# Kernel tuning notes

Measured on AMD Instinct MI355X. Metric: run time of the kernel, lower is better.

The kernel has to match this reference:

```python
import jax, jax.numpy as jnp
import numpy as np

N_CELL = 66
N_SUB = 29934
N = N_CELL + N_SUB  # 30000 nodes
F = 256
E_HALF = 480000
K = 3
LAYERS = 2
BN_EPS = 1e-5


def setup_inputs() -> dict:
    key = jax.random.key(0)
    ks = jax.random.split(key, 8)
    cell_feat = jax.random.normal(ks[0], (N_CELL, F), dtype=jnp.float32)
    sub_feat = jax.random.normal(ks[1], (N_SUB, F), dtype=jnp.float32)
    # interaction_edge builds a symmetric directed edge list: (a,b) and (b,a)
    src = jax.random.randint(ks[2], (E_HALF,), 0, N)
    dst = jax.random.randint(ks[3], (E_HALF,), 0, N)
    edge_index = jnp.stack([jnp.concatenate([src, dst]),
                            jnp.concatenate([dst, src])], axis=0)
    ew_half = jax.random.uniform(ks[4], (E_HALF,), dtype=jnp.float32, minval=0.1, maxval=1.0)
    edge_weight = jnp.concatenate([ew_half, ew_half])
    glorot = np.sqrt(6.0 / (F + F))
    W1 = jax.random.uniform(ks[5], (F, F), dtype=jnp.float32, minval=-glorot, maxval=glorot)
    W2 = jax.random.uniform(ks[6], (F, F), dtype=jnp.float32, minval=-glorot, maxval=glorot)
    b1 = jnp.zeros((F,), jnp.float32)
    b2 = jnp.zeros((F,), jnp.float32)
    prelu_w = jnp.full((F,), 0.25, jnp.float32)  # PReLU default init
    gamma = jnp.ones((F,), jnp.float32)
    beta = jnp.zeros((F,), jnp.float32)
    return {"cell_feat": cell_feat, "sub_feat": sub_feat,
            "edge_index": edge_index, "edge_weight": edge_weight,
            "W1": W1, "b1": b1, "W2": W2, "b2": b2,
            "prelu_w": prelu_w, "gamma": gamma, "beta": beta}


def _gcn_norm(edge_index, edge_weight, n):
    # SGConv's gcn_norm: add self-loops (weight 1), symmetric degree normalization
    loop = jnp.arange(n)
    row = jnp.concatenate([edge_index[0], loop])  # source j
    col = jnp.concatenate([edge_index[1], loop])  # target i
    ew = jnp.concatenate([edge_weight, jnp.ones((n,), edge_weight.dtype)])
    deg = jax.ops.segment_sum(ew, col, num_segments=n)
    dinv = jnp.where(deg > 0, jax.lax.rsqrt(deg), 0.0)
    norm = dinv[row] * ew * dinv[col]
    return row, col, norm


def _sgconv(x, row, col, norm, W, b, n):
    # K-hop propagation: x <- A_hat^K x, then linear
    for _ in range(K):
        x = jax.ops.segment_sum(norm[:, None] * x[row], col, num_segments=n)
    return x @ W.T + b


def _prelu_bn(x, prelu_w, gamma, beta):
    x = jnp.where(x >= 0, x, prelu_w * x)
    mean = jnp.mean(x, axis=0)
    var = jnp.mean(jnp.square(x - mean), axis=0)  # biased, training-mode BN
    return gamma * (x - mean) * jax.lax.rsqrt(var + BN_EPS) + beta


def reference(cell_feat, sub_feat, edge_index, edge_weight,
              W1, b1, W2, b2, prelu_w, gamma, beta):
    x = jnp.concatenate([cell_feat, sub_feat], axis=0)  # [N, F]
    n = x.shape[0]
    row, col, norm = _gcn_norm(edge_index, edge_weight, n)
    for W, b in ((W1, b1), (W2, b2)):
        x = _sgconv(x, row, col, norm, W, b, n)
        x = _prelu_bn(x, prelu_w, gamma, beta)
    return x[:N_CELL, :], x[N_CELL:, :]
```

## Files before the change

### kernel.cpp

```cpp
#include <hip/hip_runtime.h>
#include <hip/hip_bf16.h>

constexpr int NN    = 30000;
constexpr int NCELL = 66;
constexpr int NF    = 256;
constexpr int CAP   = 80;
constexpr float EPS = 1e-5f;

using bf16x8 = __attribute__((ext_vector_type(8))) short;
using f32x4  = __attribute__((ext_vector_type(4))) float;

__device__ __forceinline__ float bf2f(unsigned short u) {
    return __uint_as_float(((unsigned)u) << 16);
}
__device__ __forceinline__ unsigned short f2bf(float f) {
    __hip_bfloat16 h = __float2bfloat16(f);
    return *reinterpret_cast<unsigned short*>(&h);
}
__device__ __forceinline__ void acc8(float* acc, float4 u, float w) {
    unsigned a = __float_as_uint(u.x), b = __float_as_uint(u.y);
    unsigned c = __float_as_uint(u.z), d = __float_as_uint(u.w);
    acc[0] += w * __uint_as_float(a << 16);
    acc[1] += w * __uint_as_float(a & 0xffff0000u);
    acc[2] += w * __uint_as_float(b << 16);
    acc[3] += w * __uint_as_float(b & 0xffff0000u);
    acc[4] += w * __uint_as_float(c << 16);
    acc[5] += w * __uint_as_float(c & 0xffff0000u);
    acc[6] += w * __uint_as_float(d << 16);
    acc[7] += w * __uint_as_float(d & 0xffff0000u);
}
__device__ __forceinline__ void edge_meta(const unsigned long long* p, int& r, float& w) {
    unsigned long long v = *p;
    r = (int)(unsigned)(v & 0xffffffffull);
    w = (float)(unsigned)(v >> 32) * (1.0f / 16777216.0f);
}

__global__ void k_init(int* fill, float* sums) {
    int i = blockIdx.x * 256 + threadIdx.x;
    if (i < NN) fill[i] = 0;
    if (i < 2 * NF) sums[i] = 0.0f;
}

__global__ void k_zero_stats(float* sums) {
    int i = threadIdx.x;
    if (i < 2 * NF) sums[i] = 0.0f;
}

__global__ void k_cvtw(const float4* __restrict__ W, ushort4* __restrict__ Wh) {
    int idx = blockIdx.x * 256 + threadIdx.x;
    if (idx >= NF * NF / 4) return;
    float4 v = W[idx];
    ushort4 o;
    o.x = f2bf(v.x); o.y = f2bf(v.y); o.z = f2bf(v.z); o.w = f2bf(v.w);
    Wh[idx] = o;
}

__global__ void k_scatter(const int* __restrict__ ei, const float* __restrict__ ew,
                          int* fill, unsigned long long* __restrict__ bkt, int E) {
    int e = blockIdx.x * 256 + threadIdx.x;
    if (e >= E) return;
    int row = ei[e];
    int col = ei[E + e];
    unsigned q = __float2uint_rn(ew[e] * 16777216.0f);
    int pos = atomicAdd(&fill[col], 1);
    unsigned long long v = ((unsigned long long)q << 32) | (unsigned)row;
    __builtin_nontemporal_store(v, &bkt[(size_t)col * CAP + pos]);
}

__global__ void k_deg(const unsigned long long* __restrict__ bkt, const int* __restrict__ fill,
                      float* __restrict__ s1, float* __restrict__ s2) {
    int i = blockIdx.x * 256 + threadIdx.x;
    if (i >= NN) return;
    int cnt = fill[i];
    unsigned sq = 0;
    const unsigned long long* p = bkt + (size_t)i * CAP;
    for (int e = 0; e < cnt; e++) sq += (unsigned)(p[e] >> 32);
    float deg = 1.0f + (float)sq * (1.0f / 16777216.0f);
    float di = rsqrtf(deg);
    s2[i] = di;
    s1[i] = di * di;
}

__global__ void k_concat_h(const float4* __restrict__ cell, const float4* __restrict__ sub,
                           const float* __restrict__ dinv, ushort4* __restrict__ xh) {
    int idx = blockIdx.x * 256 + threadIdx.x;
    if (idx >= NN * (NF / 4)) return;
    const int CELL4 = NCELL * (NF / 4);
    float4 v = (idx < CELL4) ? cell[idx] : sub[idx - CELL4];
    float di = dinv[idx >> 6];
    ushort4 o;
    o.x = f2bf(v.x * di); o.y = f2bf(v.y * di);
    o.z = f2bf(v.z * di); o.w = f2bf(v.w * di);
    xh[idx] = o;
}

__global__ __launch_bounds__(256) void k_prop(const ushort* __restrict__ xin,
                                              ushort* __restrict__ xout,
                                              const int* __restrict__ fill,
                                              const unsigned long long* __restrict__ bkt,
                                              const float* __restrict__ scale) {
    int n = blockIdx.x * 4 + (threadIdx.x >> 6);
    int lane = threadIdx.x & 63;
    int half = lane >> 5;
    int fb = lane & 31;
    const float4* xrow = (const float4*)xin;
    const unsigned long long* base = bkt + (size_t)n * CAP;
    int cnt = fill[n];
    float acc[8];
    #pragma unroll
    for (int i = 0; i < 8; i++) acc[i] = 0.f;
    int steps = cnt >> 1;
    int it = 0;
    int e = half;
    for (; it + 8 <= steps; it += 8, e += 16) {
        int r0, r1, r2, r3, r4, r5, r6, r7;
        float w0, w1, w2, w3, w4, w5, w6, w7;
        edge_meta(base + e,      r0, w0);
        edge_meta(base + e + 2,  r1, w1);
        edge_meta(base + e + 4,  r2, w2);
        edge_meta(base + e + 6,  r3, w3);
        edge_meta(base + e + 8,  r4, w4);
        edge_meta(base + e + 10, r5, w5);
        edge_meta(base + e + 12, r6, w6);
        edge_meta(base + e + 14, r7, w7);
        float4 u0 = xrow[r0 * 32 + fb];
        float4 u1 = xrow[r1 * 32 + fb];
        float4 u2 = xrow[r2 * 32 + fb];
        float4 u3 = xrow[r3 * 32 + fb];
        float4 u4 = xrow[r4 * 32 + fb];
        float4 u5 = xrow[r5 * 32 + fb];
        float4 u6 = xrow[r6 * 32 + fb];
        float4 u7 = xrow[r7 * 32 + fb];
        acc8(acc, u0, w0); acc8(acc, u1, w1); acc8(acc, u2, w2); acc8(acc, u3, w3);
        acc8(acc, u4, w4); acc8(acc, u5, w5); acc8(acc, u6, w6); acc8(acc, u7, w7);
    }
    for (; it + 4 <= steps; it += 4, e += 8) {
        int r0, r1, r2, r3; float w0, w1, w2, w3;
        edge_meta(base + e,     r0, w0);
        edge_meta(base + e + 2, r1, w1);
        edge_meta(base + e + 4, r2, w2);
        edge_meta(base + e + 6, r3, w3);
        float4 u0 = xrow[r0 * 32 + fb];
        float4 u1 = xrow[r1 * 32 + fb];
        float4 u2 = xrow[r2 * 32 + fb];
        float4 u3 = xrow[r3 * 32 + fb];
        acc8(acc, u0, w0); acc8(acc, u1, w1); acc8(acc, u2, w2); acc8(acc, u3, w3);
    }
    for (; it < steps; ++it, e += 2) {
        int r0; float w0;
        edge_meta(base + e, r0, w0);
        float4 u0 = xrow[r0 * 32 + fb];
        acc8(acc, u0, w0);
    }
    if ((cnt & 1) && half == 0) {
        int r0; float w0;
        edge_meta(base + cnt - 1, r0, w0);
        float4 u0 = xrow[r0 * 32 + fb];
        acc8(acc, u0, w0);
    }
    #pragma unroll
    for (int i = 0; i < 8; i++) acc[i] += __shfl_xor(acc[i], 32);
    if (half == 0) {
        float4 u = xrow[n * 32 + fb];
        acc8(acc, u, 1.0f);
        float sc = scale[n];
        #pragma unroll
        for (int i = 0; i < 8; i++) acc[i] *= sc;
        unsigned p0 = ((unsigned)f2bf(acc[1]) << 16) | f2bf(acc[0]);
        unsigned p1 = ((unsigned)f2bf(acc[3]) << 16) | f2bf(acc[2]);
        unsigned p2 = ((unsigned)f2bf(acc[5]) << 16) | f2bf(acc[4]);
        unsigned p3 = ((unsigned)f2bf(acc[7]) << 16) | f2bf(acc[6]);
        float4 o;
        o.x = __uint_as_float(p0); o.y = __uint_as_float(p1);
        o.z = __uint_as_float(p2); o.w = __uint_as_float(p3);
        ((float4*)xout)[n * 32 + fb] = o;
    }
}

__global__ __launch_bounds__(256) void k_gemm_fused(const short* __restrict__ A,
                                                    const short* __restrict__ B,
                                                    const float* __restrict__ bias,
                                                    const float* __restrict__ pw,
                                                    float* __restrict__ y,
                                                    float* __restrict__ sums) {
    constexpr int RT = NN / 16;
    int w    = threadIdx.x >> 6;
    int lane = threadIdx.x & 63;
    int rt   = blockIdx.x * 4 + w;
    int ml   = lane & 15;
    int q    = lane >> 4;
    bool valid = rt < RT;
    __shared__ float red[2][4][NF];
    f32x4 acc[16];
    #pragma unroll
    for (int i = 0; i < 16; i++) acc[i] = (f32x4){0.f, 0.f, 0.f, 0.f};
    if (valid) {
        const short* arow = A + (rt * 16 + ml) * NF + q * 8;
        #pragma unroll
        for (int ks = 0; ks < 8; ks++) {
            bf16x8 a = *(const bf16x8*)(arow + ks * 32);
            #pragma unroll
            for (int nt = 0; nt < 16; nt++) {
                bf16x8 b = *(const bf16x8*)(B + (nt * 16 + ml) * NF + ks * 32 + q * 8);
                acc[nt] = __builtin_amdgcn_mfma_f32_16x16x32_bf16(a, b, acc[nt], 0, 0, 0);
            }
        }
    }
    #pragma unroll
    for (int nt = 0; nt < 16; nt++) {
        int col = nt * 16 + ml;
        float s = 0.f, s2 = 0.f;
        if (valid) {
            float bb = bias[col];
            float pc = pw[col];
            #pragma unroll
            for (int r = 0; r < 4; r++) {
                float v = acc[nt][r] + bb;
                v = (v >= 0.f) ? v : pc * v;
                s += v; s2 += v * v;
                y[(rt * 16 + q * 4 + r) * NF + col] = v;
            }
        }
        s  += __shfl_xor(s, 16);  s  += __shfl_xor(s, 32);
        s2 += __shfl_xor(s2, 16); s2 += __shfl_xor(s2, 32);
        if (lane < 16) { red[0][w][col] = s; red[1][w][col] = s2; }
    }
    __syncthreads();
    int t = threadIdx.x;
    float v0 = red[0][0][t] + red[0][1][t] + red[0][2][t] + red[0][3][t];
    float v1 = red[1][0][t] + red[1][1][t] + red[1][2][t] + red[1][3][t];
    atomicAdd(&sums[t], v0);
    atomicAdd(&sums[NF + t], v1);
}

__global__ void k_finalize(const float* __restrict__ sums, const float* __restrict__ gamma,
                           const float* __restrict__ beta, float* __restrict__ ss) {
    int t = threadIdx.x;
    float mean = sums[t] / (float)NN;
    float var = sums[NF + t] / (float)NN - mean * mean;
    if (var < 0.f) var = 0.f;
    float istd = rsqrtf(var + EPS);
    float sc = gamma[t] * istd;
    ss[t] = sc;
    ss[NF + t] = beta[t] - mean * sc;
}

__global__ void k_apply_h(const float4* __restrict__ y, const float* __restrict__ ss,
                          const float* __restrict__ dinv, ushort4* __restrict__ xh) {
    int idx = blockIdx.x * 256 + threadIdx.x;
    if (idx >= NN * (NF / 4)) return;
    int f = (idx & 63) * 4;
    float di = dinv[idx >> 6];
    float4 v = y[idx];
    ushort4 o;
    o.x = f2bf((v.x * ss[f]     + ss[NF + f])     * di);
    o.y = f2bf((v.y * ss[f + 1] + ss[NF + f + 1]) * di);
    o.z = f2bf((v.z * ss[f + 2] + ss[NF + f + 2]) * di);
    o.w = f2bf((v.w * ss[f + 3] + ss[NF + f + 3]) * di);
    xh[idx] = o;
}

__global__ void k_apply_out(const float4* __restrict__ y, const float* __restrict__ ss,
                            float4* __restrict__ out) {
    int idx = blockIdx.x * 256 + threadIdx.x;
    if (idx >= NN * (NF / 4)) return;
    int f = (idx & 63) * 4;
    float4 v = y[idx];
    float4 o;
    o.x = v.x * ss[f]     + ss[NF + f];
    o.y = v.y * ss[f + 1] + ss[NF + f + 1];
    o.z = v.z * ss[f + 2] + ss[NF + f + 2];
    o.w = v.w * ss[f + 3] + ss[NF + f + 3];
    out[idx] = o;
}

extern "C" void kernel_launch(void* const* d_in, const int* in_sizes, int n_in,
                              void* d_out, int out_size, void* d_ws, size_t ws_size,
                              hipStream_t stream) {
    const float* cell  = (const float*)d_in[0];
    const float* sub   = (const float*)d_in[1];
    const int*   ei    = (const int*)  d_in[2];
    const float* ew    = (const float*)d_in[3];
    const float* W1    = (const float*)d_in[4];
    const float* bias1 = (const float*)d_in[5];
    const float* W2    = (const float*)d_in[6];
    const float* bias2 = (const float*)d_in[7];
    const float* pw    = (const float*)d_in[8];
    const float* gamma = (const float*)d_in[9];
    const float* beta  = (const float*)d_in[10];
    float* out = (float*)d_out;
    const int E = in_sizes[3];

    char* ws = (char*)d_ws;
    size_t off = 0;
    auto alloc = [&](size_t bytes) -> void* {
        void* p = ws + off;
        off = (off + bytes + 255) & ~((size_t)255);
        return p;
    };
    ushort* xh0 = (ushort*)alloc((size_t)NN * NF * 2);
    ushort* xh1 = (ushort*)alloc((size_t)NN * NF * 2);
    float*  yf  = (float*) alloc((size_t)NN * NF * 4);
    ushort* W1h = (ushort*)alloc((size_t)NF * NF * 2);
    ushort* W2h = (ushort*)alloc((size_t)NF * NF * 2);
    unsigned long long* bkt = (unsigned long long*)alloc((size_t)NN * CAP * 8);
    int*    fill = (int*)  alloc((size_t)NN * 4);
    float*  s1   = (float*)alloc((size_t)NN * 4);
    float*  s2   = (float*)alloc((size_t)NN * 4);
    float*  sums = (float*)alloc((size_t)2 * NF * 4);
    float*  ss   = (float*)alloc((size_t)2 * NF * 4);

    const int gN  = (NN + 255) / 256;
    const int gE  = (E + 255) / 256;
    const int gV4 = (NN * NF / 4 + 255) / 256;
    const int gW4 = (NF * NF / 4 + 255) / 256;
    const int gP  = NN / 4;
    const int gG  = (NN / 16 + 3) / 4;

    k_init<<<gN, 256, 0, stream>>>(fill, sums);
    k_cvtw<<<gW4, 256, 0, stream>>>((const float4*)W1, (ushort4*)W1h);
    k_cvtw<<<gW4, 256, 0, stream>>>((const float4*)W2, (ushort4*)W2h);
    k_scatter<<<gE, 256, 0, stream>>>(ei, ew, fill, bkt, E);
    k_deg<<<gN, 256, 0, stream>>>(bkt, fill, s1, s2);
    k_concat_h<<<gV4, 256, 0, stream>>>((const float4*)cell, (const float4*)sub, s2, (ushort4*)xh0);

    k_prop<<<gP, 256, 0, stream>>>(xh0, xh1, fill, bkt, s1);
    k_prop<<<gP, 256, 0, stream>>>(xh1, xh0, fill, bkt, s1);
    k_prop<<<gP, 256, 0, stream>>>(xh0, xh1, fill, bkt, s2);
    k_gemm_fused<<<gG, 256, 0, stream>>>((const short*)xh1, (const short*)W1h, bias1, pw, yf, sums);
    k_finalize<<<1, 256, 0, stream>>>(sums, gamma, beta, ss);
    k_apply_h<<<gV4, 256, 0, stream>>>((const float4*)yf, ss, s2, (ushort4*)xh0);
    k_zero_stats<<<1, 512, 0, stream>>>(sums);

    k_prop<<<gP, 256, 0, stream>>>(xh0, xh1, fill, bkt, s1);
    k_prop<<<gP, 256, 0, stream>>>(xh1, xh0, fill, bkt, s1);
    k_prop<<<gP, 256, 0, stream>>>(xh0, xh1, fill, bkt, s2);
    k_gemm_fused<<<gG, 256, 0, stream>>>((const short*)xh1, (const short*)W2h, bias2, pw, yf, sums);
    k_finalize<<<1, 256, 0, stream>>>(sums, gamma, beta, ss);
    k_apply_out<<<gV4, 256, 0, stream>>>((const float4*)yf, ss, (float4*)out);
}
```

Before: 696.3 us.

## Compact padded edge buckets into packed 32-bit CSR for propagation

```diff
diff --git a/kernel.cpp b/kernel.cpp
--- a/kernel.cpp
+++ b/kernel.cpp
@@ -29,30 +29,31 @@
     acc[6] += w * __uint_as_float(d << 16);
     acc[7] += w * __uint_as_float(d & 0xffff0000u);
 }
-__device__ __forceinline__ void edge_meta(const unsigned long long* p, int& r, float& w) {
-    unsigned long long v = *p;
-    r = (int)(unsigned)(v & 0xffffffffull);
-    w = (float)(unsigned)(v >> 32) * (1.0f / 16777216.0f);
-}
-
-__global__ void k_init(int* fill, float* sums) {
+__device__ __forceinline__ void edge_meta(const unsigned* p, int& r, float& w) {
+    unsigned v = *p;
+    r = (int)(v & 0xffffu);
+    w = (float)(v >> 16) * (1.0f / 65536.0f);
+}
+
+__global__ void k_init(int* fill, float* sums, int* cursor) {
     int i = blockIdx.x * 256 + threadIdx.x;
     if (i < NN) fill[i] = 0;
     if (i < 2 * NF) sums[i] = 0.0f;
-}
-
-__global__ void k_zero_stats(float* sums) {
-    int i = threadIdx.x;
-    if (i < 2 * NF) sums[i] = 0.0f;
-}
-
-__global__ void k_cvtw(const float4* __restrict__ W, ushort4* __restrict__ Wh) {
+    if (i == 0) *cursor = 0;
+}
+
+__global__ void k_cvtw2(const float4* __restrict__ W1, const float4* __restrict__ W2,
+                        ushort4* __restrict__ W1h, ushort4* __restrict__ W2h) {
     int idx = blockIdx.x * 256 + threadIdx.x;
-    if (idx >= NF * NF / 4) return;
-    float4 v = W[idx];
+    const int NW = NF * NF / 4;
+    if (idx >= 2 * NW) return;
+    const float4* src = (idx < NW) ? W1 : W2;
+    ushort4* dst = (idx < NW) ? W1h : W2h;
+    int j = (idx < NW) ? idx : idx - NW;
+    float4 v = src[j];
     ushort4 o;
     o.x = f2bf(v.x); o.y = f2bf(v.y); o.z = f2bf(v.z); o.w = f2bf(v.w);
-    Wh[idx] = o;
+    dst[j] = o;
 }
 
 __global__ void k_scatter(const int* __restrict__ ei, const float* __restrict__ ew,
@@ -67,14 +68,27 @@
     __builtin_nontemporal_store(v, &bkt[(size_t)col * CAP + pos]);
 }
 
-__global__ void k_deg(const unsigned long long* __restrict__ bkt, const int* __restrict__ fill,
-                      float* __restrict__ s1, float* __restrict__ s2) {
+__global__ void k_compact(const unsigned long long* __restrict__ bkt,
+                          const int* __restrict__ fill,
+                          unsigned* __restrict__ csr,
+                          int* __restrict__ col_beg, int* __restrict__ col_end,
+                          float* __restrict__ s1, float* __restrict__ s2,
+                          int* cursor) {
     int i = blockIdx.x * 256 + threadIdx.x;
     if (i >= NN) return;
     int cnt = fill[i];
+    const unsigned long long* p = bkt + (size_t)i * CAP;
     unsigned sq = 0;
-    const unsigned long long* p = bkt + (size_t)i * CAP;
-    for (int e = 0; e < cnt; e++) sq += (unsigned)(p[e] >> 32);
+    int pos = atomicAdd(cursor, cnt);
+    col_beg[i] = pos;
+    col_end[i] = pos + cnt;
+    for (int e = 0; e < cnt; e++) {
+        unsigned long long v = p[e];
+        unsigned q = (unsigned)(v >> 32);
+        sq += q;
+        unsigned entry = ((q >> 8) << 16) | (unsigned)(v & 0xffffull);
+        csr[pos + e] = entry;
+    }
     float deg = 1.0f + (float)sq * (1.0f / 16777216.0f);
     float di = rsqrtf(deg);
     s2[i] = di;
@@ -96,16 +110,18 @@
 
 __global__ __launch_bounds__(256) void k_prop(const ushort* __restrict__ xin,
                                               ushort* __restrict__ xout,
-                                              const int* __restrict__ fill,
-                                              const unsigned long long* __restrict__ bkt,
+                                              const int* __restrict__ col_beg,
+                                              const int* __restrict__ col_end,
+                                              const unsigned* __restrict__ csr,
                                               const float* __restrict__ scale) {
     int n = blockIdx.x * 4 + (threadIdx.x >> 6);
     int lane = threadIdx.x & 63;
     int half = lane >> 5;
     int fb = lane & 31;
     const float4* xrow = (const float4*)xin;
-    const unsigned long long* base = bkt + (size_t)n * CAP;
-    int cnt = fill[n];
+    int beg = col_beg[n];
+    int cnt = col_end[n] - beg;
+    const unsigned* base = csr + beg;
     float acc[8];
     #pragma unroll
     for (int i = 0; i < 8; i++) acc[i] = 0.f;
@@ -233,7 +249,7 @@
     atomicAdd(&sums[NF + t], v1);
 }
 
-__global__ void k_finalize(const float* __restrict__ sums, const float* __restrict__ gamma,
+__global__ void k_finalize(float* __restrict__ sums, const float* __restrict__ gamma,
                            const float* __restrict__ beta, float* __restrict__ ss) {
     int t = threadIdx.x;
     float mean = sums[t] / (float)NN;
@@ -243,6 +259,8 @@
     float sc = gamma[t] * istd;
     ss[t] = sc;
     ss[NF + t] = beta[t] - mean * sc;
+    sums[t] = 0.0f;
+    sums[NF + t] = 0.0f;
 }
 
 __global__ void k_apply_h(const float4* __restrict__ y, const float* __restrict__ ss,
@@ -304,37 +322,40 @@
     ushort* W1h = (ushort*)alloc((size_t)NF * NF * 2);
     ushort* W2h = (ushort*)alloc((size_t)NF * NF * 2);
     unsigned long long* bkt = (unsigned long long*)alloc((size_t)NN * CAP * 8);
+    unsigned* csr = (unsigned*)alloc((size_t)E * 4);
+    int*    col_beg = (int*)alloc((size_t)NN * 4);
+    int*    col_end = (int*)alloc((size_t)NN * 4);
     int*    fill = (int*)  alloc((size_t)NN * 4);
     float*  s1   = (float*)alloc((size_t)NN * 4);
     float*  s2   = (float*)alloc((size_t)NN * 4);
     float*  sums = (float*)alloc((size_t)2 * NF * 4);
     float*  ss   = (float*)alloc((size_t)2 * NF * 4);
+    int*    cursor = (int*)alloc(64);
 
     const int gN  = (NN + 255) / 256;
     const int gE  = (E + 255) / 256;
     const int gV4 = (NN * NF / 4 + 255) / 256;
-    const int gW4 = (NF * NF / 4 + 255) / 256;
+    const int gW2 = (2 * NF * NF / 4 + 255) / 256;
     const int gP  = NN / 4;
     const int gG  = (NN / 16 + 3) / 4;
 
-    k_init<<<gN, 256, 0, stream>>>(fill, sums);
-    k_cvtw<<<gW4, 256, 0, stream>>>((const float4*)W1, (ushort4*)W1h);
-    k_cvtw<<<gW4, 256, 0, stream>>>((const float4*)W2, (ushort4*)W2h);
+    k_init<<<gN, 256, 0, stream>>>(fill, sums, cursor);
+    k_cvtw2<<<gW2, 256, 0, stream>>>((const float4*)W1, (const float4*)W2,
+                                     (ushort4*)W1h, (ushort4*)W2h);
     k_scatter<<<gE, 256, 0, stream>>>(ei, ew, fill, bkt, E);
-    k_deg<<<gN, 256, 0, stream>>>(bkt, fill, s1, s2);
+    k_compact<<<gN, 256, 0, stream>>>(bkt, fill, csr, col_beg, col_end, s1, s2, cursor);
     k_concat_h<<<gV4, 256, 0, stream>>>((const float4*)cell, (const float4*)sub, s2, (ushort4*)xh0);
 
-    k_prop<<<gP, 256, 0, stream>>>(xh0, xh1, fill, bkt, s1);
-    k_prop<<<gP, 256, 0, stream>>>(xh1, xh0, fill, bkt, s1);
-    k_prop<<<gP, 256, 0, stream>>>(xh0, xh1, fill, bkt, s2);
+    k_prop<<<gP, 256, 0, stream>>>(xh0, xh1, col_beg, col_end, csr, s1);
+    k_prop<<<gP, 256, 0, stream>>>(xh1, xh0, col_beg, col_end, csr, s1);
+    k_prop<<<gP, 256, 0, stream>>>(xh0, xh1, col_beg, col_end, csr, s2);
     k_gemm_fused<<<gG, 256, 0, stream>>>((const short*)xh1, (const short*)W1h, bias1, pw, yf, sums);
     k_finalize<<<1, 256, 0, stream>>>(sums, gamma, beta, ss);
     k_apply_h<<<gV4, 256, 0, stream>>>((const float4*)yf, ss, s2, (ushort4*)xh0);
-    k_zero_stats<<<1, 512, 0, stream>>>(sums);
-
-    k_prop<<<gP, 256, 0, stream>>>(xh0, xh1, fill, bkt, s1);
-    k_prop<<<gP, 256, 0, stream>>>(xh1, xh0, fill, bkt, s1);
-    k_prop<<<gP, 256, 0, stream>>>(xh0, xh1, fill, bkt, s2);
+
+    k_prop<<<gP, 256, 0, stream>>>(xh0, xh1, col_beg, col_end, csr, s1);
+    k_prop<<<gP, 256, 0, stream>>>(xh1, xh0, col_beg, col_end, csr, s1);
+    k_prop<<<gP, 256, 0, stream>>>(xh0, xh1, col_beg, col_end, csr, s2);
     k_gemm_fused<<<gG, 256, 0, stream>>>((const short*)xh1, (const short*)W2h, bias2, pw, yf, sums);
     k_finalize<<<1, 256, 0, stream>>>(sums, gamma, beta, ss);
     k_apply_out<<<gV4, 256, 0, stream>>>((const float4*)yf, ss, (float4*)out);
```

Result: faster. 673.2 us (-3.3%).
